# Optimization experiments

Hardware: AMD Instinct MI355X
Metric: run time of the kernel (lower is better)

Reference implementation:

```python
import jax, jax.numpy as jnp
import numpy as np

SEQ_LEN = 2048   # configs.seq_len == h == KFSSM H
PRED_LEN = 720   # configs.pred_len == p
D_MODEL = 128    # configs.d_model == KFSSM N (complex state size N//2)
C_OUT = 64       # configs.c_out == channel dim of u
BATCH = 128


def setup_inputs() -> dict:
    key = jax.random.key(0)
    ks = jax.random.split(key, 12)
    H, n2, p = SEQ_LEN, D_MODEL // 2, PRED_LEN
    u = jax.random.normal(ks[0], (BATCH, SEQ_LEN, C_OUT), jnp.float32)
    x_mark_enc = jax.random.normal(ks[1], (BATCH, SEQ_LEN, 4), jnp.float32)
    x_dec = jax.random.normal(ks[2], (BATCH, PRED_LEN, C_OUT), jnp.float32)
    x_mark_dec = jax.random.normal(ks[3], (BATCH, PRED_LEN, 4), jnp.float32)
    # standard-normal noise; scaled by learned std inside reference (matches torch.normal(0, std))
    W_noise = jax.random.normal(ks[4], (BATCH, SEQ_LEN, C_OUT), jnp.float32)
    # Model params
    D = jax.random.normal(ks[5], (H,), jnp.float32)
    log_variance = jnp.log(1.0 + jax.random.uniform(ks[6], (1,), jnp.float32))
    # KFSSM params
    C_param = jax.random.normal(ks[7], (H, n2, 2), jnp.float32)  # view_as_real of complex C
    log_dt = (jax.random.uniform(ks[8], (H,), jnp.float32)
              * (np.log(0.1) - np.log(0.001)) + np.log(0.001))
    log_A_real = jnp.log(0.5 * jnp.ones((H, n2), jnp.float32))
    A_imag = np.pi * jnp.tile(jnp.arange(n2, dtype=jnp.float32)[None, :], (H, 1))
    # outporj: Linear(h -> 2p) then GLU(dim=2)
    proj_w = jax.random.normal(ks[9], (2 * p, H), jnp.float32) * 0.02
    proj_b = jnp.zeros((2 * p,), jnp.float32)
    return dict(u=u, x_mark_enc=x_mark_enc, x_dec=x_dec, x_mark_dec=x_mark_dec,
                W_noise=W_noise, D=D, log_variance=log_variance, C_param=C_param,
                log_dt=log_dt, log_A_real=log_A_real, A_imag=A_imag,
                proj_w=proj_w, proj_b=proj_b)


def _ssm_kernels(Nl, C_param, log_dt, log_A_real, A_imag):
    # KFSSM.forward(N=Nl): returns K, K2 of shape (H, Nl)
    dt = jnp.exp(log_dt)                              # (H,)
    C = C_param[..., 0] + 1j * C_param[..., 1]        # (H, n2)
    A = -jnp.exp(log_A_real) + 1j * A_imag            # (H, n2)
    ar = jnp.arange(Nl, dtype=log_dt.dtype)
    Bk = A[:, :1] * ar[None, :] * dt[:, None]         # (H, Nl) complex
    dtA = A * dt[:, None]                             # (H, n2)
    Kexp = jnp.exp(dtA[:, :, None] * ar[None, None, :])  # (H, n2, Nl)
    Cc = C * (jnp.exp(dtA) - 1.0) / A                 # (H, n2)
    K = 2.0 * jnp.einsum('hn,hnl->hl', Cc, Kexp).real # (H, Nl)
    K2 = 2.0 * (K * Bk).real                          # (H, Nl)
    return K, K2


def reference(u, x_mark_enc, x_dec, x_mark_dec, W_noise, D, log_variance,
              C_param, log_dt, log_A_real, A_imag, proj_w, proj_b):
    # instance normalization over time
    x_mean = jnp.mean(u, axis=1, keepdims=True)                  # (B,1,N)
    u0 = u - x_mean
    x_var = jnp.var(u0, axis=1, ddof=1, keepdims=True) + 1e-5    # unbiased, as torch.var
    un = u0 / jnp.sqrt(x_var)
    # Kalman process noise
    std = jnp.sqrt(jnp.exp(log_variance))                        # (1,)
    W = std * W_noise                                            # (B,L,N)
    l, Nch = un.shape[1], un.shape[2]
    nfft = 2 * l
    K, K2 = _ssm_kernels(Nch, C_param, log_dt, log_A_real, A_imag)  # (H=l, Nch)
    k_f = jnp.fft.rfft(K.T, n=nfft, axis=-1)                     # (Nch, l+1)
    k2_f = jnp.fft.rfft(K2.T, n=nfft, axis=-1)
    u_f = jnp.fft.rfft(jnp.transpose(un, (0, 2, 1)), n=nfft, axis=-1)   # (B,Nch,l+1)
    w_f = jnp.fft.rfft(jnp.transpose(W, (0, 2, 1)), n=nfft, axis=-1)
    y = (jnp.fft.irfft(u_f * k2_f, n=nfft, axis=-1)
         + jnp.fft.irfft(w_f * k_f, n=nfft, axis=-1))            # (B,Nch,2l)
    y = jnp.transpose(y, (0, 2, 1))[:, -l:, :] + un * D[:, None] # (B,l,Nch)
    # outporj: Linear(h->2p) over time axis, then GLU(dim=2); Dropout1d is identity at eval
    z = jnp.einsum('bnh,ph->bnp', jnp.transpose(y, (0, 2, 1)), proj_w) + proj_b  # (B,Nch,2p)
    a, b = jnp.split(z, 2, axis=2)
    y = jnp.transpose(a * jax.nn.sigmoid(b), (0, 2, 1))          # (B,p,Nch)
    y = y * jnp.sqrt(x_var) + x_mean
    return y[:, -PRED_LEN:, :]
```

## Files before the change

### kernel.cpp

```cpp
#include <hip/hip_runtime.h>
#include <math.h>

typedef unsigned short u16;
typedef unsigned int u32;
typedef __attribute__((ext_vector_type(8))) short short8;
typedef __attribute__((ext_vector_type(4))) float f32x4;

#define B_   128
#define L_   2048
#define C_   64
#define P_   720
#define P2_  1440
#define NPAD 1536
#define NFFT 4096
#define NROW (B_*C_)
#define TCHUNK 16

__device__ __forceinline__ u16 f2bf(float f) {
  union { float f; unsigned u; } x; x.f = f;
  unsigned r = x.u + 0x7fffu + ((x.u >> 16) & 1u);
  return (u16)(r >> 16);
}
__device__ __forceinline__ float bf2f_lo(u32 v) {
  union { unsigned u; float f; } x; x.u = v << 16; return x.f;
}
__device__ __forceinline__ float bf2f_hi(u32 v) {
  union { unsigned u; float f; } x; x.u = v & 0xffff0000u; return x.f;
}

__device__ __forceinline__ float2 cmul(float2 a, float2 b) {
  return make_float2(a.x * b.x - a.y * b.y, a.x * b.y + a.y * b.x);
}
__device__ __forceinline__ float2 cadd(float2 a, float2 b) { return make_float2(a.x + b.x, a.y + b.y); }
__device__ __forceinline__ float2 csub(float2 a, float2 b) { return make_float2(a.x - b.x, a.y - b.y); }

#define CSWAP(i, j) { float2 tt = a[i]; a[i] = a[j]; a[j] = tt; }

template<bool INV, bool HZ>
__device__ __forceinline__ void dft16(float2 a[16]) {
  const float S  = INV ? 1.f : -1.f;
  const float c1 = 0.9238795325112867f, s1 = 0.3826834323650898f, q2 = 0.7071067811865476f;
  const float2 W1 = make_float2( c1, S * s1), W2 = make_float2( q2, S * q2), W3 = make_float2( s1, S * c1);
  const float2 W5 = make_float2(-s1, S * c1), W6 = make_float2(-q2, S * q2), W7 = make_float2(-c1, S * s1);
  if (HZ) {
    a[8]  = a[0];
    a[9]  = cmul(a[1], W1);
    a[10] = cmul(a[2], W2);
    a[11] = cmul(a[3], W3);
    a[12] = make_float2(-S * a[4].y, S * a[4].x);
    a[13] = cmul(a[5], W5);
    a[14] = cmul(a[6], W6);
    a[15] = cmul(a[7], W7);
  } else {
    float2 t;
    t = csub(a[0], a[8]);  a[0] = cadd(a[0], a[8]);  a[8]  = t;
    t = csub(a[1], a[9]);  a[1] = cadd(a[1], a[9]);  a[9]  = cmul(t, W1);
    t = csub(a[2], a[10]); a[2] = cadd(a[2], a[10]); a[10] = cmul(t, W2);
    t = csub(a[3], a[11]); a[3] = cadd(a[3], a[11]); a[11] = cmul(t, W3);
    t = csub(a[4], a[12]); a[4] = cadd(a[4], a[12]); a[12] = make_float2(-S * t.y, S * t.x);
    t = csub(a[5], a[13]); a[5] = cadd(a[5], a[13]); a[13] = cmul(t, W5);
    t = csub(a[6], a[14]); a[6] = cadd(a[6], a[14]); a[14] = cmul(t, W6);
    t = csub(a[7], a[15]); a[7] = cadd(a[7], a[15]); a[15] = cmul(t, W7);
  }
#pragma unroll
  for (int h = 0; h < 16; h += 8) {
    float2 t;
    t = csub(a[h+0], a[h+4]); a[h+0] = cadd(a[h+0], a[h+4]); a[h+4] = t;
    t = csub(a[h+1], a[h+5]); a[h+1] = cadd(a[h+1], a[h+5]); a[h+5] = cmul(t, W2);
    t = csub(a[h+2], a[h+6]); a[h+2] = cadd(a[h+2], a[h+6]); a[h+6] = make_float2(-S * t.y, S * t.x);
    t = csub(a[h+3], a[h+7]); a[h+3] = cadd(a[h+3], a[h+7]); a[h+7] = cmul(t, W6);
  }
#pragma unroll
  for (int q = 0; q < 16; q += 4) {
    float2 t;
    t = csub(a[q+0], a[q+2]); a[q+0] = cadd(a[q+0], a[q+2]); a[q+2] = t;
    t = csub(a[q+1], a[q+3]); a[q+1] = cadd(a[q+1], a[q+3]); a[q+3] = make_float2(-S * t.y, S * t.x);
  }
#pragma unroll
  for (int p = 0; p < 16; p += 2) {
    float2 t = csub(a[p], a[p+1]); a[p] = cadd(a[p], a[p+1]); a[p+1] = t;
  }
  CSWAP(1, 8); CSWAP(2, 4); CSWAP(3, 12); CSWAP(5, 10); CSWAP(7, 14); CSWAP(11, 13);
}

__device__ __forceinline__ void twchain(float2 a[16], float2 w1) {
  float2 w2 = cmul(w1, w1);
  float2 w3 = cmul(w2, w1);
  float2 w4 = cmul(w2, w2);
  float2 w5 = cmul(w3, w2);
  float2 w6 = cmul(w3, w3);
  float2 w7 = cmul(w4, w3);
  float2 w8 = cmul(w4, w4);
  float2 w9 = cmul(w5, w4);
  float2 w10 = cmul(w5, w5);
  float2 w11 = cmul(w6, w5);
  float2 w12 = cmul(w6, w6);
  float2 w13 = cmul(w7, w6);
  float2 w14 = cmul(w7, w7);
  float2 w15 = cmul(w8, w7);
  a[1]  = cmul(a[1],  w1);  a[2]  = cmul(a[2],  w2);  a[3]  = cmul(a[3],  w3);
  a[4]  = cmul(a[4],  w4);  a[5]  = cmul(a[5],  w5);  a[6]  = cmul(a[6],  w6);
  a[7]  = cmul(a[7],  w7);  a[8]  = cmul(a[8],  w8);  a[9]  = cmul(a[9],  w9);
  a[10] = cmul(a[10], w10); a[11] = cmul(a[11], w11); a[12] = cmul(a[12], w12);
  a[13] = cmul(a[13], w13); a[14] = cmul(a[14], w14); a[15] = cmul(a[15], w15);
}

__device__ __forceinline__ void lds_wA(float2* X, const float2 r[16], int tid) {
  int base = (tid & 15) * 16 + ((tid >> 4) ^ ((tid & 7) << 1));
#pragma unroll
  for (int i = 0; i < 16; ++i) X[base + i * 256] = r[i];
}
__device__ __forceinline__ void lds_wB(float2* X, const float2 r[16], int tid) {
#pragma unroll
  for (int i = 0; i < 16; ++i)
    X[((tid & 0xF0) + i) * 16 + ((tid & 15) ^ ((i & 7) << 1))] = r[i];
}
__device__ __forceinline__ void lds_rd(const float2* X, float2 r[16], int tid) {
  const float4* X4 = (const float4*)X;
#pragma unroll
  for (int p = 0; p < 8; ++p) {
    float4 v = X4[tid * 8 + (p ^ (tid & 7))];
    r[2 * p]     = make_float2(v.x, v.y);
    r[2 * p + 1] = make_float2(v.z, v.w);
  }
}

__device__ __forceinline__ void fft_fwd_hz(float2 r[16], float2* X, int tid, const float2* twg) {
  dft16<false, true>(r);
  twchain(r, twg[tid]);
  lds_wA(X, r, tid);
  __syncthreads();
  lds_rd(X, r, tid);
  dft16<false, false>(r);
  twchain(r, twg[(tid & 15) << 4]);
  __syncthreads();
  lds_wB(X, r, tid);
  __syncthreads();
  lds_rd(X, r, tid);
  dft16<false, false>(r);
}

__device__ __forceinline__ void fft_inv(float2 r[16], float2* X, int tid, const float2* twg) {
  dft16<true, false>(r);
  __syncthreads();
  lds_wB(X, r, tid);
  __syncthreads();
  lds_rd(X, r, tid);
  float2 wb = twg[(tid & 15) << 4];
  twchain(r, make_float2(wb.x, -wb.y));
  dft16<true, false>(r);
  __syncthreads();
  lds_wA(X, r, tid);
  __syncthreads();
  lds_rd(X, r, tid);
  float2 wa = twg[tid];
  twchain(r, make_float2(wa.x, -wa.y));
  dft16<true, false>(r);
}

__global__ void k_twfill(float2* __restrict__ tw) {
  int k = threadIdx.x;
  double ang = -2.0 * 3.14159265358979323846 * (double)k / 4096.0;
  tw[k] = make_float2((float)cos(ang), (float)sin(ang));
}

__global__ void k_wconv(const float* __restrict__ pw, u16* __restrict__ wb) {
  size_t idx = (size_t)blockIdx.x * 256 + threadIdx.x;
  int n = (int)(idx >> 11);
  int k = (int)(idx & 2047);
  float v = (n < P2_) ? pw[(size_t)n * L_ + k] : 0.0f;
  wb[idx] = f2bf(v);
}

__global__ __launch_bounds__(256) void k_stats1(const float* __restrict__ u, float* __restrict__ ps,
                                                float* __restrict__ pq) {
  int blk = blockIdx.x;
  int b = blk >> 4, q = blk & 15;
  int tid = threadIdx.x;
  int c4 = tid & 15, g = tid >> 4;
  const float4* u4 = (const float4*)(u + ((size_t)b * L_ + q * 128) * C_);
  float4 s = make_float4(0.f, 0.f, 0.f, 0.f), sq = s;
#pragma unroll
  for (int i = 0; i < 8; ++i) {
    float4 v = u4[(size_t)(g + 16 * i) * 16 + c4];
    s.x += v.x; s.y += v.y; s.z += v.z; s.w += v.w;
    sq.x += v.x * v.x; sq.y += v.y * v.y; sq.z += v.z * v.z; sq.w += v.w * v.w;
  }
  __shared__ float4 sb[16][16], qb[16][16];
  sb[g][c4] = s; qb[g][c4] = sq;
  __syncthreads();
  if (g == 0) {
    float4 S = sb[0][c4], Q = qb[0][c4];
#pragma unroll
    for (int k = 1; k < 16; ++k) {
      float4 a = sb[k][c4], d = qb[k][c4];
      S.x += a.x; S.y += a.y; S.z += a.z; S.w += a.w;
      Q.x += d.x; Q.y += d.y; Q.z += d.z; Q.w += d.w;
    }
    ((float4*)ps)[blk * 16 + c4] = S;
    ((float4*)pq)[blk * 16 + c4] = Q;
  }
}

__global__ __launch_bounds__(256) void k_stats2(const float* __restrict__ ps, const float* __restrict__ pq,
                                                float4* __restrict__ mv) {
  int gid = blockIdx.x * 256 + threadIdx.x;
  int b = gid >> 6, c = gid & 63;
  float S = 0.f, Q = 0.f;
#pragma unroll
  for (int q = 0; q < 16; ++q) {
    S += ps[(size_t)(b * 16 + q) * 64 + c];
    Q += pq[(size_t)(b * 16 + q) * 64 + c];
  }
  float mean = S * (1.0f / 2048.0f);
  float var = (Q - S * S * (1.0f / 2048.0f)) * (1.0f / 2047.0f) + 1e-5f;
  float sv = sqrtf(var);
  mv[gid] = make_float4(mean, sv, 1.0f / sv, 0.0f);
}

__global__ __launch_bounds__(256) void k_ssmk(const float* __restrict__ Cp, const float* __restrict__ ldt,
                                              const float* __restrict__ lAr, const float* __restrict__ Aim,
                                              float2* __restrict__ kz) {
  int gid = blockIdx.x * 256 + threadIdx.x;
  int h = gid & 2047;
  int j = gid >> 11;
  float dt = expf(ldt[h]);
  float accx = 0.f;
  float Ar0 = 0.f;
  for (int n = 0; n < 64; ++n) {
    float Ar = -expf(lAr[h * 64 + n]);
    float Ai = Aim[h * 64 + n];
    if (n == 0) Ar0 = Ar;
    float dAr = Ar * dt, dAi = Ai * dt;
    float er = expf(dAr);
    float s1, c1; sincosf(dAi, &s1, &c1);
    float emr = er * c1 - 1.0f, emi = er * s1;
    float inv = 1.0f / (Ar * Ar + Ai * Ai);
    float qr = (emr * Ar + emi * Ai) * inv;
    float qi = (emi * Ar - emr * Ai) * inv;
    float cr = Cp[(size_t)(h * 64 + n) * 2];
    float ci = Cp[(size_t)(h * 64 + n) * 2 + 1];
    float ccr = cr * qr - ci * qi;
    float cci = cr * qi + ci * qr;
    float ej = expf(dAr * (float)j);
    float sj, cj; sincosf(dAi * (float)j, &sj, &cj);
    accx += ccr * (ej * cj) - cci * (ej * sj);
  }
  float K = 2.0f * accx;
  float K2 = 2.0f * K * (Ar0 * (float)j * dt);
  kz[(size_t)j * L_ + h] = make_float2(K2, -K);
}

__global__ __launch_bounds__(256) void k_packT(const float* __restrict__ u, const float* __restrict__ Wn,
                                               const float* __restrict__ lv, const float4* __restrict__ mv,
                                               u32* __restrict__ zu) {
  int b = blockIdx.x >> 5;
  int t0 = (blockIdx.x & 31) << 6;
  int tid = threadIdx.x;
  float stdn = sqrtf(__expf(lv[0]));
  __shared__ float2 tile[64][65];
  int c = tid & 63, r = tid >> 6;
  float4 m = mv[b * C_ + c];
#pragma unroll
  for (int i = 0; i < 16; ++i) {
    int t = t0 + i * 4 + r;
    size_t idx = ((size_t)b * L_ + t) * C_ + c;
    float uu = (u[idx] - m.x) * m.z;
    float ww = Wn[idx] * stdn;
    tile[i * 4 + r][c] = make_float2(uu, ww);
  }
  __syncthreads();
  int t = tid & 63, cb = tid >> 6;
#pragma unroll
  for (int i = 0; i < 16; ++i) {
    int c2 = i * 4 + cb;
    float2 v = tile[t][c2];
    zu[((size_t)(b * C_ + c2)) * L_ + t0 + t] = ((u32)f2bf(v.y) << 16) | (u32)f2bf(v.x);
  }
}

__global__ __launch_bounds__(256) void k_fftk(const float2* __restrict__ kz, const float2* __restrict__ twg,
                                              float2* __restrict__ G) {
  __shared__ float2 X[NFFT];
  int j = blockIdx.x, tid = threadIdx.x;
  float2 r[16];
#pragma unroll
  for (int n2 = 0; n2 < 8; ++n2) r[n2] = kz[(size_t)j * L_ + n2 * 256 + tid];
  fft_fwd_hz(r, X, tid, twg);
  const float sc = 1.0f / 4096.0f;
#pragma unroll
  for (int k0 = 0; k0 < 16; ++k0)
    G[(size_t)j * NFFT + k0 * 256 + tid] = make_float2(r[k0].x * sc, r[k0].y * sc);
}

__global__ __launch_bounds__(256) void k_fftmain(const u32* __restrict__ zu, const float2* __restrict__ twg,
                                                 const float2* __restrict__ G, const float* __restrict__ Dv,
                                                 u16* __restrict__ yT) {
  __shared__ float2 X[NFFT];
  int row = blockIdx.x;
  int j = row & 63;
  int tid = threadIdx.x;
  float2 r[16];
  float usav[8];
#pragma unroll
  for (int n2 = 0; n2 < 8; ++n2) {
    u32 v = zu[(size_t)row * L_ + n2 * 256 + tid];
    float uu = bf2f_lo(v), ww = bf2f_hi(v);
    r[n2] = make_float2(uu, ww);
    usav[n2] = uu;
  }
  fft_fwd_hz(r, X, tid, twg);
  const float2* Gj = G + (size_t)j * NFFT;
#pragma unroll
  for (int k0 = 0; k0 < 16; ++k0) r[k0] = cmul(r[k0], Gj[k0 * 256 + tid]);
  fft_inv(r, X, tid, twg);
#pragma unroll
  for (int n2 = 8; n2 < 16; ++n2) {
    int t = (n2 - 8) * 256 + tid;
    float yv = r[n2].x + usav[n2 - 8] * Dv[t];
    yT[(size_t)row * L_ + t] = f2bf(yv);
  }
}

__device__ __forceinline__ int lds_ix(int row, int slot) {
  return row * 32 + ((slot ^ ((row >> 1) & 3)) << 3);
}

__global__ __launch_bounds__(256) void k_gemm(const u16* __restrict__ A, const u16* __restrict__ B,
                                              float* __restrict__ Cmat) {
  __shared__ u16 As[128 * 32];
  __shared__ u16 Bs[128 * 32];
  const int K = L_, N = NPAD;
  int tid = threadIdx.x;
  int bid = blockIdx.x;
  int swz = (bid & 7) * 96 + (bid >> 3);
  int bm = swz % 64, bn = swz / 64;
  int wave = tid >> 6, lane = tid & 63;
  int wm = (wave >> 1) << 6, wn = (wave & 1) << 6;
  int lr = lane & 15, lk = lane >> 4;
  int trow = tid >> 2, tslot = tid & 3;
  const u16* Ag = A + (size_t)(bm * 128 + trow) * K + tslot * 8;
  const u16* Bg = B + (size_t)(bn * 128 + trow) * K + tslot * 8;
  f32x4 acc[4][4] = {};
  uint4 pa0 = *(const uint4*)(Ag);
  uint4 pa1 = *(const uint4*)(Ag + (size_t)64 * K);
  uint4 pb0 = *(const uint4*)(Bg);
  uint4 pb1 = *(const uint4*)(Bg + (size_t)64 * K);
  for (int kt = 0; kt < K; kt += 32) {
    __syncthreads();
    *(uint4*)&As[lds_ix(trow, tslot)] = pa0;
    *(uint4*)&As[lds_ix(trow + 64, tslot)] = pa1;
    *(uint4*)&Bs[lds_ix(trow, tslot)] = pb0;
    *(uint4*)&Bs[lds_ix(trow + 64, tslot)] = pb1;
    __syncthreads();
    if (kt + 32 < K) {
      pa0 = *(const uint4*)(Ag + kt + 32);
      pa1 = *(const uint4*)(Ag + (size_t)64 * K + kt + 32);
      pb0 = *(const uint4*)(Bg + kt + 32);
      pb1 = *(const uint4*)(Bg + (size_t)64 * K + kt + 32);
    }
    short8 af[4], bf[4];
#pragma unroll
    for (int i2 = 0; i2 < 4; ++i2) af[i2] = *(const short8*)&As[lds_ix(wm + i2 * 16 + lr, lk)];
#pragma unroll
    for (int j2 = 0; j2 < 4; ++j2) bf[j2] = *(const short8*)&Bs[lds_ix(wn + j2 * 16 + lr, lk)];
#pragma unroll
    for (int i2 = 0; i2 < 4; ++i2)
#pragma unroll
      for (int j2 = 0; j2 < 4; ++j2)
        acc[i2][j2] = __builtin_amdgcn_mfma_f32_16x16x32_bf16(af[i2], bf[j2], acc[i2][j2], 0, 0, 0);
  }
#pragma unroll
  for (int i2 = 0; i2 < 4; ++i2)
#pragma unroll
    for (int j2 = 0; j2 < 4; ++j2)
#pragma unroll
      for (int r = 0; r < 4; ++r)
        Cmat[(size_t)(bm * 128 + wm + i2 * 16 + lk * 4 + r) * N + bn * 128 + wn + j2 * 16 + lr] =
            acc[i2][j2][r];
}

__global__ __launch_bounds__(256) void k_epi(const float* __restrict__ z, const float* __restrict__ pb,
                                             const float4* __restrict__ mv, float* __restrict__ out) {
  int b = blockIdx.x / 23;
  int p0 = (blockIdx.x % 23) * 32;
  int tid = threadIdx.x;
  __shared__ float tile[64][33];
  int pp = tid & 31, ci = tid >> 5;
  for (int cc = ci; cc < 64; cc += 8) {
    int p = p0 + pp;
    float val = 0.f;
    if (p < P_) {
      size_t rowb = (size_t)(b * C_ + cc) * NPAD;
      float a = z[rowb + p] + pb[p];
      float g = z[rowb + P_ + p] + pb[P_ + p];
      float4 m = mv[b * C_ + cc];
      val = a * (1.0f / (1.0f + __expf(-g))) * m.y + m.x;
    }
    tile[cc][pp] = val;
  }
  __syncthreads();
  int c2 = tid & 63, pi = tid >> 6;
  for (int q = pi; q < 32; q += 4) {
    int p = p0 + q;
    if (p < P_) out[((size_t)b * P_ + p) * C_ + c2] = tile[c2][q];
  }
}

extern "C" void kernel_launch(void* const* d_in, const int* in_sizes, int n_in,
                              void* d_out, int out_size, void* d_ws, size_t ws_size,
                              hipStream_t stream) {
  const float* u   = (const float*)d_in[0];
  const float* Wn  = (const float*)d_in[4];
  const float* Dv  = (const float*)d_in[5];
  const float* lv  = (const float*)d_in[6];
  const float* Cp  = (const float*)d_in[7];
  const float* ldt = (const float*)d_in[8];
  const float* lAr = (const float*)d_in[9];
  const float* Aim = (const float*)d_in[10];
  const float* pw  = (const float*)d_in[11];
  const float* pb  = (const float*)d_in[12];
  float* out = (float*)d_out;
  char* ws = (char*)d_ws;

  float2* tw = (float2*)(ws + 0);
  float4* mv = (float4*)(ws + (64 << 10));
  float2* G  = (float2*)(ws + (1 << 20));
  float2* kz = (float2*)(ws + (3 << 20));
  u16*    Wb = (u16*)   (ws + (4 << 20));
  float*  ps = (float*) (ws + (10 << 20));
  float*  pq = (float*) (ws + (10 << 20) + (512 << 10));
  u16*    yT = (u16*)   (ws + (16 << 20));
  u32*    zu = (u32*)   (ws + ((size_t)48 << 20));
  float*  zz = (float*) (ws + ((size_t)112 << 20));

  k_twfill<<<1, 256, 0, stream>>>(tw);
  k_wconv<<<(NPAD * L_) / 256, 256, 0, stream>>>(pw, Wb);
  k_stats1<<<B_ * TCHUNK, 256, 0, stream>>>(u, ps, pq);
  k_stats2<<<(B_ * C_) / 256, 256, 0, stream>>>(ps, pq, mv);
  k_ssmk<<<(C_ * L_) / 256, 256, 0, stream>>>(Cp, ldt, lAr, Aim, kz);
  k_packT<<<B_ * (L_ / 64), 256, 0, stream>>>(u, Wn, lv, mv, zu);
  k_fftk<<<C_, 256, 0, stream>>>(kz, tw, G);
  k_fftmain<<<NROW, 256, 0, stream>>>(zu, tw, G, Dv, yT);
  k_gemm<<<64 * (NPAD / 128), 256, 0, stream>>>(yT, Wb, zz);
  k_epi<<<B_ * 23, 256, 0, stream>>>(zz, pb, mv, out);
}
```

Before: 353.8 us.

## Pack two channel rows into one inverse FFT using real-output symmetry

Each block now handles two channel rows. It does two forward FFTs, then merges the two spectral products into one complex spectrum whose inverse has row1's result in the real part and row2's in the imaginary part, using Hermitian-symmetry reconstruction through shared memory. This halves the number of inverse FFTs and the grid size. The cost is extra register pressure (Y1, usav2), extra shared-memory passes and syncs, and a rescaled kernel spectrum (1/8192) to account for the combination factor.

```diff
diff --git a/kernel.cpp b/kernel.cpp
--- a/kernel.cpp
+++ b/kernel.cpp
@@ -287,7 +287,7 @@
 #pragma unroll
   for (int n2 = 0; n2 < 8; ++n2) r[n2] = kz[(size_t)j * L_ + n2 * 256 + tid];
   fft_fwd_hz(r, X, tid, twg);
-  const float sc = 1.0f / 4096.0f;
+  const float sc = 1.0f / 8192.0f;
 #pragma unroll
   for (int k0 = 0; k0 < 16; ++k0)
     G[(size_t)j * NFFT + k0 * 256 + tid] = make_float2(r[k0].x * sc, r[k0].y * sc);
@@ -297,28 +297,56 @@
                                                  const float2* __restrict__ G, const float* __restrict__ Dv,
                                                  u16* __restrict__ yT) {
   __shared__ float2 X[NFFT];
-  int row = blockIdx.x;
-  int j = row & 63;
+  int pair = blockIdx.x;
+  int b = pair >> 5, j1 = pair & 31, j2 = j1 + 32;
+  int row1 = b * 64 + j1, row2 = b * 64 + j2;
   int tid = threadIdx.x;
-  float2 r[16];
-  float usav[8];
+  float2 r[16], Y1[16];
+  float usav1[8], usav2[8];
 #pragma unroll
   for (int n2 = 0; n2 < 8; ++n2) {
-    u32 v = zu[(size_t)row * L_ + n2 * 256 + tid];
-    float uu = bf2f_lo(v), ww = bf2f_hi(v);
-    r[n2] = make_float2(uu, ww);
-    usav[n2] = uu;
+    u32 v = zu[(size_t)row1 * L_ + n2 * 256 + tid];
+    r[n2] = make_float2(bf2f_lo(v), bf2f_hi(v));
+    usav1[n2] = r[n2].x;
   }
   fft_fwd_hz(r, X, tid, twg);
-  const float2* Gj = G + (size_t)j * NFFT;
-#pragma unroll
-  for (int k0 = 0; k0 < 16; ++k0) r[k0] = cmul(r[k0], Gj[k0 * 256 + tid]);
+  const float2* G1 = G + (size_t)j1 * NFFT;
+#pragma unroll
+  for (int k0 = 0; k0 < 16; ++k0) Y1[k0] = cmul(r[k0], G1[k0 * 256 + tid]);
+  __syncthreads();
+#pragma unroll
+  for (int n2 = 0; n2 < 8; ++n2) {
+    u32 v = zu[(size_t)row2 * L_ + n2 * 256 + tid];
+    r[n2] = make_float2(bf2f_lo(v), bf2f_hi(v));
+    usav2[n2] = r[n2].x;
+  }
+  fft_fwd_hz(r, X, tid, twg);
+  const float2* G2 = G + (size_t)j2 * NFFT;
+#pragma unroll
+  for (int k0 = 0; k0 < 16; ++k0) r[k0] = cmul(r[k0], G2[k0 * 256 + tid]);
+  __syncthreads();
+  int rr = (tid & 15) * 16 + (tid >> 4);
+  int wsw = ((rr & 15) << 4) | (rr >> 4);
+  int rp = (tid == 0) ? 0 : 256 - rr;
+  int rsw = ((rp & 15) << 4) | (rp >> 4);
+#pragma unroll
+  for (int k0 = 0; k0 < 16; ++k0) {
+    X[k0 * 256 + wsw] = make_float2(Y1[k0].x + r[k0].y, r[k0].x - Y1[k0].y);
+  }
+  __syncthreads();
+#pragma unroll
+  for (int k0 = 0; k0 < 16; ++k0) {
+    int k0p = (tid == 0) ? ((16 - k0) & 15) : (15 - k0);
+    float2 Tm = X[k0p * 256 + rsw];
+    r[k0] = make_float2(Y1[k0].x - r[k0].y + Tm.x, Y1[k0].y + r[k0].x + Tm.y);
+  }
   fft_inv(r, X, tid, twg);
 #pragma unroll
   for (int n2 = 8; n2 < 16; ++n2) {
     int t = (n2 - 8) * 256 + tid;
-    float yv = r[n2].x + usav[n2 - 8] * Dv[t];
-    yT[(size_t)row * L_ + t] = f2bf(yv);
+    float d = Dv[t];
+    yT[(size_t)row1 * L_ + t] = f2bf(r[n2].x + usav1[n2 - 8] * d);
+    yT[(size_t)row2 * L_ + t] = f2bf(r[n2].y + usav2[n2 - 8] * d);
   }
 }
 
@@ -441,7 +469,7 @@
   k_ssmk<<<(C_ * L_) / 256, 256, 0, stream>>>(Cp, ldt, lAr, Aim, kz);
   k_packT<<<B_ * (L_ / 64), 256, 0, stream>>>(u, Wn, lv, mv, zu);
   k_fftk<<<C_, 256, 0, stream>>>(kz, tw, G);
-  k_fftmain<<<NROW, 256, 0, stream>>>(zu, tw, G, Dv, yT);
+  k_fftmain<<<NROW / 2, 256, 0, stream>>>(zu, tw, G, Dv, yT);
   k_gemm<<<64 * (NPAD / 128), 256, 0, stream>>>(yT, Wb, zz);
   k_epi<<<B_ * 23, 256, 0, stream>>>(zz, pb, mv, out);
 }
```

After: 344.7 us. 1.03x faster.
